# Kernel optimization log

Hardware: AMD Instinct MI355X
Metric: run time of the kernel (lower is better)

The kernel has to match this reference:

```python
import jax, jax.numpy as jnp
import numpy as np

VOCAB = 100000
EMB = 128
B = 16384
C = 20
N = 20


def setup_inputs() -> dict:
    key = jax.random.key(0)
    k1, k2, k3, k4, k5 = jax.random.split(key, 5)
    initrange = 1.0 / EMB
    return {
        "pos_target": jax.random.randint(k1, (B,), 0, VOCAB),
        "pos_contexts": jax.random.randint(k2, (B, C), 0, VOCAB),
        "pos_negatives": jax.random.randint(k3, (B, N), 0, VOCAB),
        "context_table": jax.random.uniform(k4, (VOCAB, EMB), jnp.float32, -initrange, initrange),
        "output_table": jax.random.uniform(k5, (VOCAB, EMB), jnp.float32, -initrange, initrange),
    }


def reference(pos_target, pos_contexts, pos_negatives, context_table, output_table):
    # gather + sum over context window: [B, C, D] -> [B, D]
    mean_contexts = jnp.sum(context_table[pos_contexts], axis=1)
    emb_target = output_table[pos_target]           # [B, D]
    emb_negs = output_table[pos_negatives]          # [B, N, D]

    # positive objective: dot(mean_contexts, emb_target) per row
    pos_score = jnp.clip(jnp.sum(mean_contexts * emb_target, axis=1), -10.0, 10.0)
    objective = -jax.nn.log_sigmoid(pos_score)      # [B]

    # negative objective: bmm [B,N,D] x [B,D] -> [B,N]
    neg_score = jnp.clip(jnp.einsum("bnd,bd->bn", emb_negs, mean_contexts), -10.0, 10.0)
    neg_objective = -jnp.sum(jax.nn.log_sigmoid(-neg_score), axis=1)  # [B]

    return jnp.mean(objective + neg_objective)
```

## Files before the change

### kernel.cpp

```cpp
#include <hip/hip_runtime.h>
#include <math.h>

#define VOCAB 100000
#define EMB   128
#define BATCH 16384
#define CTX   20
#define NEG   20
#define NSCORE (NEG + 1)

__device__ __forceinline__ float dot4(float4 a, float4 b) {
    return fmaf(a.x, b.x, fmaf(a.y, b.y, fmaf(a.z, b.z, a.w * b.w)));
}

__device__ __forceinline__ float fast_softplus(float x) {
    return __logf(1.0f + __expf(x));
}

__global__ __launch_bounds__(256, 4) void cbow_loss_kernel(
    const int*   __restrict__ pos_target,
    const int*   __restrict__ pos_contexts,
    const int*   __restrict__ pos_negatives,
    const float* __restrict__ context_table,
    const float* __restrict__ output_table,
    float*       __restrict__ out)
{
    const int tid  = threadIdx.x;
    const int lane = tid & 63;
    const int wave = tid >> 6;
    const int q    = lane >> 4;
    const int sub  = lane & 15;

    const int row = blockIdx.x * 16 + wave * 4 + q;

    const float4* ctab = (const float4*)context_table;
    const float4* otab = (const float4*)output_table;

    int cidx0 = pos_contexts[row * CTX + sub];
    int cidx1 = (sub < CTX - 16) ? pos_contexts[row * CTX + 16 + sub] : 0;
    int sidx0 = (sub == 0) ? pos_target[row]
                           : pos_negatives[row * NEG + sub - 1];
    int sidx1 = (sub < NSCORE - 16) ? pos_negatives[row * NEG + 15 + sub] : 0;

    auto ctx_idx = [&](int j) {
        return (j < 16) ? __shfl(cidx0, j, 16) : __shfl(cidx1, j - 16, 16);
    };
    auto sc_idx = [&](int j) {
        return (j < 16) ? __shfl(sidx0, j, 16) : __shfl(sidx1, j - 16, 16);
    };

    float4 alo = make_float4(0.f, 0.f, 0.f, 0.f);
    float4 ahi = make_float4(0.f, 0.f, 0.f, 0.f);
    {
        float4 lo[2][5], hi[2][5];
#pragma unroll
        for (int j = 0; j < 5; ++j) {
            const int idx = ctx_idx(j);
            lo[0][j] = ctab[idx * 32 + sub];
            hi[0][j] = ctab[idx * 32 + 16 + sub];
        }
#pragma unroll
        for (int g = 0; g < 4; ++g) {
            if (g + 1 < 4) {
#pragma unroll
                for (int j = 0; j < 5; ++j) {
                    const int idx = ctx_idx((g + 1) * 5 + j);
                    lo[(g + 1) & 1][j] = ctab[idx * 32 + sub];
                    hi[(g + 1) & 1][j] = ctab[idx * 32 + 16 + sub];
                }
            }
#pragma unroll
            for (int j = 0; j < 5; ++j) {
                const float4 a = lo[g & 1][j], b = hi[g & 1][j];
                alo.x += a.x; alo.y += a.y; alo.z += a.z; alo.w += a.w;
                ahi.x += b.x; ahi.y += b.y; ahi.z += b.z; ahi.w += b.w;
            }
        }
    }

    float part[NSCORE];
    {
        float4 slo[2][7], shi[2][7];
#pragma unroll
        for (int j = 0; j < 7; ++j) {
            const int idx = sc_idx(j);
            slo[0][j] = otab[idx * 32 + sub];
            shi[0][j] = otab[idx * 32 + 16 + sub];
        }
#pragma unroll
        for (int g = 0; g < 3; ++g) {
            if (g + 1 < 3) {
#pragma unroll
                for (int j = 0; j < 7; ++j) {
                    const int idx = sc_idx((g + 1) * 7 + j);
                    slo[(g + 1) & 1][j] = otab[idx * 32 + sub];
                    shi[(g + 1) & 1][j] = otab[idx * 32 + 16 + sub];
                }
            }
#pragma unroll
            for (int j = 0; j < 7; ++j) {
                part[g * 7 + j] =
                    dot4(alo, slo[g & 1][j]) + dot4(ahi, shi[g & 1][j]);
            }
        }
    }

#pragma unroll
    for (int s = 8; s >= 1; s >>= 1) {
#pragma unroll
        for (int n = 0; n < NSCORE; ++n) part[n] += __shfl_xor(part[n], s);
    }

    float ps = fminf(fmaxf(part[0], -10.f), 10.f);
    float loss = fast_softplus(-ps);
#pragma unroll
    for (int n = 1; n < NSCORE; ++n) {
        float ns = fminf(fmaxf(part[n], -10.f), 10.f);
        loss += fast_softplus(ns);
    }

    __shared__ float sdata[16];
    if (sub == 0) sdata[wave * 4 + q] = loss;
    __syncthreads();
    if (tid == 0) {
        float s = 0.f;
#pragma unroll
        for (int i = 0; i < 16; ++i) s += sdata[i];
        atomicAdd(out, s * (1.0f / (float)BATCH));
    }
}

extern "C" void kernel_launch(void* const* d_in, const int* in_sizes, int n_in,
                              void* d_out, int out_size, void* d_ws, size_t ws_size,
                              hipStream_t stream) {
    const int*   pos_target    = (const int*)d_in[0];
    const int*   pos_contexts  = (const int*)d_in[1];
    const int*   pos_negatives = (const int*)d_in[2];
    const float* context_table = (const float*)d_in[3];
    const float* output_table  = (const float*)d_in[4];
    float* out = (float*)d_out;

    hipMemsetAsync(out, 0, sizeof(float), stream);

    const int rows_per_block = 16;
    const int grid = BATCH / rows_per_block;
    cbow_loss_kernel<<<grid, 256, 0, stream>>>(
        pos_target, pos_contexts, pos_negatives, context_table, output_table, out);
}
```

Measured before the change: 150.9 us.

## Use 32 lanes per batch row instead of 16 and raise occupancy target

Result: slower. 168.9 us (+11.9%).

```diff
diff --git a/kernel.cpp b/kernel.cpp
--- a/kernel.cpp
+++ b/kernel.cpp
@@ -16,7 +16,7 @@
     return __logf(1.0f + __expf(x));
 }
 
-__global__ __launch_bounds__(256, 4) void cbow_loss_kernel(
+__global__ __launch_bounds__(256, 8) void cbow_loss_kernel(
     const int*   __restrict__ pos_target,
     const int*   __restrict__ pos_contexts,
     const int*   __restrict__ pos_negatives,
@@ -27,104 +27,84 @@
     const int tid  = threadIdx.x;
     const int lane = tid & 63;
     const int wave = tid >> 6;
-    const int q    = lane >> 4;
-    const int sub  = lane & 15;
+    const int half = lane >> 5;
+    const int sub  = lane & 31;
 
-    const int row = blockIdx.x * 16 + wave * 4 + q;
+    const int row = blockIdx.x * 8 + wave * 2 + half;
 
     const float4* ctab = (const float4*)context_table;
     const float4* otab = (const float4*)output_table;
 
-    int cidx0 = pos_contexts[row * CTX + sub];
-    int cidx1 = (sub < CTX - 16) ? pos_contexts[row * CTX + 16 + sub] : 0;
-    int sidx0 = (sub == 0) ? pos_target[row]
-                           : pos_negatives[row * NEG + sub - 1];
-    int sidx1 = (sub < NSCORE - 16) ? pos_negatives[row * NEG + 15 + sub] : 0;
+    int cidx = (sub < CTX) ? pos_contexts[row * CTX + sub] : 0;
+    int sidx = (sub == 0) ? pos_target[row]
+             : (sub <= NEG ? pos_negatives[row * NEG + sub - 1] : 0);
 
-    auto ctx_idx = [&](int j) {
-        return (j < 16) ? __shfl(cidx0, j, 16) : __shfl(cidx1, j - 16, 16);
-    };
-    auto sc_idx = [&](int j) {
-        return (j < 16) ? __shfl(sidx0, j, 16) : __shfl(sidx1, j - 16, 16);
-    };
+    auto ctx_idx = [&](int j) { return __shfl(cidx, j, 32); };
+    auto sc_idx  = [&](int j) { return __shfl(sidx, j, 32); };
 
-    float4 alo = make_float4(0.f, 0.f, 0.f, 0.f);
-    float4 ahi = make_float4(0.f, 0.f, 0.f, 0.f);
+    float4 acc = make_float4(0.f, 0.f, 0.f, 0.f);
     {
-        float4 lo[2][5], hi[2][5];
+        float4 buf[2][5];
 #pragma unroll
-        for (int j = 0; j < 5; ++j) {
-            const int idx = ctx_idx(j);
-            lo[0][j] = ctab[idx * 32 + sub];
-            hi[0][j] = ctab[idx * 32 + 16 + sub];
-        }
+        for (int j = 0; j < 5; ++j)
+            buf[0][j] = ctab[ctx_idx(j) * 32 + sub];
 #pragma unroll
         for (int g = 0; g < 4; ++g) {
             if (g + 1 < 4) {
 #pragma unroll
-                for (int j = 0; j < 5; ++j) {
-                    const int idx = ctx_idx((g + 1) * 5 + j);
-                    lo[(g + 1) & 1][j] = ctab[idx * 32 + sub];
-                    hi[(g + 1) & 1][j] = ctab[idx * 32 + 16 + sub];
-                }
+                for (int j = 0; j < 5; ++j)
+                    buf[(g + 1) & 1][j] = ctab[ctx_idx((g + 1) * 5 + j) * 32 + sub];
             }
 #pragma unroll
             for (int j = 0; j < 5; ++j) {
-                const float4 a = lo[g & 1][j], b = hi[g & 1][j];
-                alo.x += a.x; alo.y += a.y; alo.z += a.z; alo.w += a.w;
-                ahi.x += b.x; ahi.y += b.y; ahi.z += b.z; ahi.w += b.w;
+                const float4 a = buf[g & 1][j];
+                acc.x += a.x; acc.y += a.y; acc.z += a.z; acc.w += a.w;
             }
         }
     }
 
     float part[NSCORE];
     {
-        float4 slo[2][7], shi[2][7];
+        float4 sbuf[2][7];
 #pragma unroll
-        for (int j = 0; j < 7; ++j) {
-            const int idx = sc_idx(j);
-            slo[0][j] = otab[idx * 32 + sub];
-            shi[0][j] = otab[idx * 32 + 16 + sub];
-        }
+        for (int j = 0; j < 7; ++j)
+            sbuf[0][j] = otab[sc_idx(j) * 32 + sub];
 #pragma unroll
         for (int g = 0; g < 3; ++g) {
             if (g + 1 < 3) {
 #pragma unroll
-                for (int j = 0; j < 7; ++j) {
-                    const int idx = sc_idx((g + 1) * 7 + j);
-                    slo[(g + 1) & 1][j] = otab[idx * 32 + sub];
-                    shi[(g + 1) & 1][j] = otab[idx * 32 + 16 + sub];
-                }
+                for (int j = 0; j < 7; ++j)
+                    sbuf[(g + 1) & 1][j] = otab[sc_idx((g + 1) * 7 + j) * 32 + sub];
             }
 #pragma unroll
-            for (int j = 0; j < 7; ++j) {
-                part[g * 7 + j] =
-                    dot4(alo, slo[g & 1][j]) + dot4(ahi, shi[g & 1][j]);
-            }
+            for (int j = 0; j < 7; ++j)
+                part[g * 7 + j] = dot4(acc, sbuf[g & 1][j]);
         }
     }
 
 #pragma unroll
-    for (int s = 8; s >= 1; s >>= 1) {
+    for (int s = 16; s >= 1; s >>= 1) {
 #pragma unroll
         for (int n = 0; n < NSCORE; ++n) part[n] += __shfl_xor(part[n], s);
     }
 
-    float ps = fminf(fmaxf(part[0], -10.f), 10.f);
-    float loss = fast_softplus(-ps);
+    __shared__ float sdata[8];
+    if (sub == 0) {
+        float ps = fminf(fmaxf(part[0], -10.f), 10.f);
+        float loss = fast_softplus(-ps);
 #pragma unroll
-    for (int n = 1; n < NSCORE; ++n) {
-        float ns = fminf(fmaxf(part[n], -10.f), 10.f);
-        loss += fast_softplus(ns);
+        for (int n = 1; n < NSCORE; ++n) {
+            float ns = fminf(fmaxf(part[n], -10.f), 10.f);
+            loss += fast_softplus(ns);
+        }
+        sdata[wave * 2 + half] = loss;
     }
+    __syncthreads();
 
-    __shared__ float sdata[16];
-    if (sub == 0) sdata[wave * 4 + q] = loss;
-    __syncthreads();
     if (tid == 0) {
         float s = 0.f;
 #pragma unroll
-        for (int i = 0; i < 16; ++i) s += sdata[i];
+        for (int i = 0; i < 8; ++i) s += sdata[i];
         atomicAdd(out, s * (1.0f / (float)BATCH));
     }
 }
@@ -141,7 +121,7 @@
 
     hipMemsetAsync(out, 0, sizeof(float), stream);
 
-    const int rows_per_block = 16;
+    const int rows_per_block = 8;
     const int grid = BATCH / rows_per_block;
     cbow_loss_kernel<<<grid, 256, 0, stream>>>(
         pos_target, pos_contexts, pos_negatives, context_table, output_table, out);
```
